# Performance work log

Hardware: AMD Instinct MI355X
Metric: run time of the kernel (lower is better)

The kernel has to match this reference:

```python
import jax, jax.numpy as jnp
import numpy as np

TAU = 2.0
V_TH = 1.0
ALPHA = 2.0  # ATan surrogate alpha (spikingjelly default)

@jax.custom_vjp
def atan_heaviside(x):
    # Forward: Heaviside spike; backward: ATan surrogate gradient.
    return (x >= 0).astype(x.dtype)

def _atan_fwd(x):
    return atan_heaviside(x), x

def _atan_bwd(x, g):
    sg = (ALPHA / 2.0) / (1.0 + (jnp.pi / 2.0 * ALPHA * x) ** 2)
    return (g * sg,)

atan_heaviside.defvjp(_atan_fwd, _atan_bwd)

def lif_scan(cur):
    # cur: [T, B, F] input currents. LIF: H = V + (X - V)/tau; S = H >= v_th; hard reset V = H*(1-S).
    def step(v, x_t):
        h = v + (x_t - v) / TAU
        s = atan_heaviside(h - V_TH)
        v_new = h * (1.0 - s)
        return v_new, s
    v0 = jnp.zeros(cur.shape[1:], dtype=cur.dtype)
    _, spikes = jax.lax.scan(step, v0, cur)
    return spikes

def setup_inputs() -> dict:
    key = jax.random.key(0)
    k1, k2 = jax.random.split(key)
    T, B, F_in, F_out = 64, 256, 1024, 1024
    x = jax.random.normal(k1, (T, B, F_in), dtype=jnp.float32)
    W = jax.random.normal(k2, (F_out, F_in), dtype=jnp.float32) * (1.0 / np.sqrt(F_in))
    return {"x": x, "W": W}

def reference(x, W):
    # Linear projection over all timesteps, then multi-step LIF recurrence.
    cur = jnp.einsum('tbf,of->tbo', x, W)  # [T, B, F_out]
    return lif_scan(cur)
```

## Files before the change

kernel.cpp:

```cpp
#include <hip/hip_runtime.h>


#define T_DIM 64
#define B_DIM 256
#define F_DIM 1024
#define K_DIM 1024
#define M_DIM 16384
#define COLS  (B_DIM * F_DIM)
#define KP    2048
#define MARGIN 6e-5f
#define LIST_CAP 32768

typedef __attribute__((ext_vector_type(8))) short short8;
typedef __attribute__((ext_vector_type(4))) float floatx4;

#define ASYNC_CP16(gp, lp)                                                     \
    __builtin_amdgcn_global_load_lds(                                          \
        (const __attribute__((address_space(1))) unsigned int*)(gp),           \
        (__attribute__((address_space(3))) unsigned int*)(lp), 16, 0, 0)

__device__ inline unsigned short f32_to_bf16_rne(float f) {
    unsigned int u = __builtin_bit_cast(unsigned int, f);
    unsigned int r = (u + 0x7FFFu + ((u >> 16) & 1u)) >> 16;
    return (unsigned short)r;
}
__device__ inline float bf16_to_f32(unsigned short h) {
    unsigned int u = ((unsigned int)h) << 16;
    return __builtin_bit_cast(float, u);
}

__global__ __launch_bounds__(256) void split_kernel(
    const float* __restrict__ x, const float* __restrict__ Wm,
    unsigned short* __restrict__ A, unsigned short* __restrict__ B,
    unsigned int* __restrict__ counter)
{
    if (blockIdx.x == 0 && threadIdx.x == 0) *counter = 0;
    const int blk = blockIdx.x;
    const float* in;
    unsigned short* dst;
    int g;
    int orow;
    if (blk < 16384) {
        g = blk * 256 + threadIdx.x;
        int e = g * 4;
        int row = e >> 10;
        orow = ((row & 255) << 6) | (row >> 8);
        in = x; dst = A;
    } else {
        g = (blk - 16384) * 256 + threadIdx.x;
        int e = g * 4;
        orow = e >> 10;
        in = Wm; dst = B;
    }
    int k = (g * 4) & 1023;
    float4 v = reinterpret_cast<const float4*>(in)[g];
    ushort4 h, l;
    float f;
    f = v.x; h.x = f32_to_bf16_rne(f); l.x = f32_to_bf16_rne(f - bf16_to_f32(h.x));
    f = v.y; h.y = f32_to_bf16_rne(f); l.y = f32_to_bf16_rne(f - bf16_to_f32(h.y));
    f = v.z; h.z = f32_to_bf16_rne(f); l.z = f32_to_bf16_rne(f - bf16_to_f32(h.z));
    f = v.w; h.w = f32_to_bf16_rne(f); l.w = f32_to_bf16_rne(f - bf16_to_f32(h.w));
    reinterpret_cast<ushort4*>(dst)[(size_t)orow * (KP / 4) + (k >> 2)] = h;
    reinterpret_cast<ushort4*>(dst)[(size_t)orow * (KP / 4) + 256 + (k >> 2)] = l;
}

__global__ __launch_bounds__(256, 2) void gemm_scan_kernel(
    const unsigned short* __restrict__ A,
    const unsigned short* __restrict__ B,
    float* __restrict__ out,
    unsigned int* __restrict__ counter, unsigned int* __restrict__ list)
{
    __shared__ unsigned short As[128 * 32];
    __shared__ unsigned short Bs[256 * 32];

    const int tid  = threadIdx.x;
    const int lane = tid & 63;
    const int wv   = tid >> 6;
    const int lid = blockIdx.x;
    const int mt  = ((lid & 7) << 4) | (lid >> 5);
    const int nt  = (lid >> 3) & 3;
    const int m0  = mt * 128;
    const int n0  = nt * 256;
    const int wm  = (wv & 1) * 64;
    const int wn  = (wv >> 1) * 128;

    floatx4 acc[4][8] = {};

    const int srow = tid >> 2;
    const int slin = (tid & 3) * 8;
    const int ssw  = (((tid & 3) ^ ((tid >> 3) & 3)) * 8);
    const int lrow = lane & 15;
    const int q    = lane >> 4;
    const int rsw  = (lrow >> 1) & 3;

    const unsigned short* Ab = A + (size_t)m0 * KP;
    const unsigned short* Bb = B + (size_t)n0 * KP;

    for (int k0 = 0; k0 < 3072; k0 += 32) {
        const int aoff = (k0 < 2048) ? k0 : k0 - 2048;
        const int boff = (k0 < 1024) ? k0 : k0 - 1024;
        __syncthreads();
        ASYNC_CP16(Ab + (size_t)srow * KP + aoff + ssw,         As + srow * 32 + slin);
        ASYNC_CP16(Ab + (size_t)(srow + 64) * KP + aoff + ssw,  As + (srow + 64) * 32 + slin);
        ASYNC_CP16(Bb + (size_t)srow * KP + boff + ssw,         Bs + srow * 32 + slin);
        ASYNC_CP16(Bb + (size_t)(srow + 64) * KP + boff + ssw,  Bs + (srow + 64) * 32 + slin);
        ASYNC_CP16(Bb + (size_t)(srow + 128) * KP + boff + ssw, Bs + (srow + 128) * 32 + slin);
        ASYNC_CP16(Bb + (size_t)(srow + 192) * KP + boff + ssw, Bs + (srow + 192) * 32 + slin);
        __syncthreads();

        const int sl = (q ^ rsw) * 8;
        short8 a[4], b[8];
#pragma unroll
        for (int i = 0; i < 4; ++i)
            a[i] = *reinterpret_cast<const short8*>(&As[(wm + i * 16 + lrow) * 32 + sl]);
#pragma unroll
        for (int j = 0; j < 8; ++j)
            b[j] = *reinterpret_cast<const short8*>(&Bs[(wn + j * 16 + lrow) * 32 + sl]);
#pragma unroll
        for (int i = 0; i < 4; ++i)
#pragma unroll
            for (int j = 0; j < 8; ++j)
                acc[i][j] = __builtin_amdgcn_mfma_f32_16x16x32_bf16(a[i], b[j], acc[i][j], 0, 0, 0);
    }

    const int col = lane & 15;
    const int b_g = mt * 2 + (wv & 1);

    unsigned int fmask = 0;
#pragma unroll
    for (int j = 0; j < 8; ++j) {
        float v = 0.f;
        bool fl = false;
#pragma unroll
        for (int i = 0; i < 4; ++i) {
#pragma unroll
            for (int qq = 0; qq < 4; ++qq) {
                if (q == qq) {
#pragma unroll
                    for (int r = 0; r < 4; ++r) {
                        float cu = acc[i][j][r];
                        float h = v + (cu - v) * 0.5f;
                        float d = h - 1.0f;
                        bool sp = (d >= 0.f);
                        fl |= (fabsf(d) < MARGIN);
                        acc[i][j][r] = sp ? 1.0f : 0.0f;
                        v = sp ? 0.f : h;
                    }
                }
                v = __shfl(v, qq * 16 + col, 64);
            }
        }
        if (fl) fmask |= (1u << j);
    }
    fmask |= __shfl_xor(fmask, 16, 64);
    fmask |= __shfl_xor(fmask, 32, 64);

    float* outp = out + (size_t)b_g * F_DIM;
#pragma unroll
    for (int i = 0; i < 4; ++i)
#pragma unroll
        for (int j = 0; j < 8; ++j)
#pragma unroll
            for (int r = 0; r < 4; ++r) {
                int t = i * 16 + q * 4 + r;
                int o = n0 + wn + j * 16 + col;
                outp[(size_t)t * COLS + o] = acc[i][j][r];
            }

    if (q == 0 && fmask) {
        for (int j = 0; j < 8; ++j)
            if (fmask & (1u << j)) {
                unsigned int idx = atomicAdd(counter, 1u);
                if (idx < LIST_CAP)
                    list[idx] = (unsigned int)((b_g << 10) | (n0 + wn + j * 16 + col));
            }
    }
}

__global__ __launch_bounds__(256) void fixup_kernel(
    const float* __restrict__ x, const float* __restrict__ W,
    const unsigned int* __restrict__ counter, const unsigned int* __restrict__ list,
    float* __restrict__ out)
{
    __shared__ double curd[T_DIM];
    __shared__ float wrow[K_DIM];
    unsigned int n = *counter;
    if (n > LIST_CAP) n = LIST_CAP;
    const int wv = threadIdx.x >> 6, lane = threadIdx.x & 63;

    for (unsigned int idx = blockIdx.x; idx < n; idx += gridDim.x) {
        const unsigned int c = list[idx];
        const int b = c >> 10, o = c & 1023;
        __syncthreads();
        for (int k = threadIdx.x; k < K_DIM; k += 256) wrow[k] = W[(size_t)o * K_DIM + k];
        __syncthreads();
        for (int it = 0; it < 16; ++it) {
            const int t = it * 4 + wv;
            const float* xp = x + (size_t)t * COLS + (size_t)b * F_DIM + lane * 16;
            double s = 0.0;
#pragma unroll
            for (int qq = 0; qq < 4; ++qq) {
                float4 xv = reinterpret_cast<const float4*>(xp)[qq];
                float4 wq = *reinterpret_cast<const float4*>(&wrow[lane * 16 + qq * 4]);
                s += (double)xv.x * (double)wq.x + (double)xv.y * (double)wq.y +
                     (double)xv.z * (double)wq.z + (double)xv.w * (double)wq.w;
            }
#pragma unroll
            for (int off = 32; off > 0; off >>= 1) s += __shfl_down(s, off, 64);
            if (lane == 0) curd[t] = s;
        }
        __syncthreads();
        if (threadIdx.x == 0) {
            double v = 0.0;
            for (int t = 0; t < T_DIM; ++t) {
                double h = v + (curd[t] - v) * 0.5;
                bool s = (h >= 1.0);
                out[(size_t)t * COLS + c] = s ? 1.0f : 0.0f;
                v = s ? 0.0 : h;
            }
        }
        __syncthreads();
    }
}

#define TILE 64
#define KC 32
#define XS_LD 36
#define SC_LD 65

__global__ __launch_bounds__(256) void lif_fused_kernel(
    const float* __restrict__ x, const float* __restrict__ Wm, float* __restrict__ out)
{
    __shared__ __align__(16) unsigned char smem_raw[TILE * SC_LD * sizeof(double)];
    float* sf = reinterpret_cast<float*>(smem_raw);
    double* sd = reinterpret_cast<double*>(smem_raw);
    float* Xs = sf;
    float* Ws = sf + TILE * XS_LD;

    const int b = blockIdx.y;
    const int o0 = blockIdx.x * TILE;
    const int tid = threadIdx.x;
    const int tx = tid & 15, ty = tid >> 4;

    double acc[4][4];
#pragma unroll
    for (int i = 0; i < 4; ++i)
#pragma unroll
        for (int j = 0; j < 4; ++j) acc[i][j] = 0.0;

    const int r = tid >> 3, c4 = (tid & 7) * 4;
    const float* xbase = x + (size_t)b * F_DIM;

    for (int k0 = 0; k0 < K_DIM; k0 += KC) {
        __syncthreads();
        float4 xv0 = *reinterpret_cast<const float4*>(xbase + (size_t)r * COLS + k0 + c4);
        float4 xv1 = *reinterpret_cast<const float4*>(xbase + (size_t)(r + 32) * COLS + k0 + c4);
        *reinterpret_cast<float4*>(Xs + r * XS_LD + c4) = xv0;
        *reinterpret_cast<float4*>(Xs + (r + 32) * XS_LD + c4) = xv1;
        float4 wv0 = *reinterpret_cast<const float4*>(Wm + (size_t)(o0 + r) * K_DIM + k0 + c4);
        float4 wv1 = *reinterpret_cast<const float4*>(Wm + (size_t)(o0 + r + 32) * K_DIM + k0 + c4);
        *reinterpret_cast<float4*>(Ws + r * XS_LD + c4) = wv0;
        *reinterpret_cast<float4*>(Ws + (r + 32) * XS_LD + c4) = wv1;
        __syncthreads();
#pragma unroll 4
        for (int kk = 0; kk < KC; ++kk) {
            double xa[4], wb[4];
#pragma unroll
            for (int i = 0; i < 4; ++i) xa[i] = (double)Xs[(4 * ty + i) * XS_LD + kk];
#pragma unroll
            for (int j = 0; j < 4; ++j) wb[j] = (double)Ws[(4 * tx + j) * XS_LD + kk];
#pragma unroll
            for (int i = 0; i < 4; ++i)
#pragma unroll
                for (int j = 0; j < 4; ++j) acc[i][j] = fma(xa[i], wb[j], acc[i][j]);
        }
    }
    __syncthreads();
#pragma unroll
    for (int i = 0; i < 4; ++i)
#pragma unroll
        for (int j = 0; j < 4; ++j) sd[(4 * ty + i) * SC_LD + (4 * tx + j)] = acc[i][j];
    __syncthreads();
    if (tid < TILE) {
        double v = 0.0;
        float* outp = out + (size_t)b * F_DIM + o0 + tid;
        for (int t = 0; t < T_DIM; ++t) {
            double cu = sd[t * SC_LD + tid];
            double h = v + (cu - v) * 0.5;
            bool s = (h >= 1.0);
            outp[(size_t)t * COLS] = s ? 1.0f : 0.0f;
            v = s ? 0.0 : h;
        }
    }
}

extern "C" void kernel_launch(void* const* d_in, const int* in_sizes, int n_in,
                              void* d_out, int out_size, void* d_ws, size_t ws_size,
                              hipStream_t stream) {
    const float* x = (const float*)d_in[0];
    const float* Wm = (const float*)d_in[1];
    float* out = (float*)d_out;

    const size_t OFF_A   = 0;
    const size_t OFF_B   = OFF_A + (size_t)M_DIM * KP * 2;
    const size_t OFF_CNT = OFF_B + (size_t)F_DIM * KP * 2;
    const size_t OFF_LST = OFF_CNT + 256;
    const size_t NEEDED  = OFF_LST + (size_t)LIST_CAP * 4;

    if (ws_size < NEEDED) {
        dim3 grid(F_DIM / TILE, B_DIM, 1);
        lif_fused_kernel<<<grid, dim3(256), 0, stream>>>(x, Wm, out);
        return;
    }

    unsigned char* ws = (unsigned char*)d_ws;
    unsigned short* Abuf = (unsigned short*)(ws + OFF_A);
    unsigned short* Bbuf = (unsigned short*)(ws + OFF_B);
    unsigned int* counter = (unsigned int*)(ws + OFF_CNT);
    unsigned int* list = (unsigned int*)(ws + OFF_LST);

    split_kernel<<<dim3(16384 + 1024), dim3(256), 0, stream>>>(x, Wm, Abuf, Bbuf, counter);
    gemm_scan_kernel<<<dim3(512), dim3(256), 0, stream>>>(Abuf, Bbuf, out, counter, list);
    fixup_kernel<<<dim3(512), dim3(256), 0, stream>>>(x, Wm, counter, list, out);
}
```

Baseline: 247.9 us.

## Load hi/lo bf16 splits together per K-step to reuse tiles across 3 MFMA passes

The split-bf16 GEMM used to run three separate K sweeps (hi*hi, lo*hi, hi*lo), reloading tiles each time. It now loads the hi and lo halves of A and B into separate LDS buffers in one 1024-long K loop and issues all three MFMA products per step. This cuts the number of K iterations and barriers and reuses each loaded tile across products. In exchange it doubles LDS use per block and raises register pressure, which could hurt occupancy at launch_bounds(256,2).

New measurement: 225.9 us. -8.9%, faster.

```diff
diff --git a/kernel.cpp b/kernel.cpp
--- a/kernel.cpp
+++ b/kernel.cpp
@@ -70,8 +70,10 @@
     float* __restrict__ out,
     unsigned int* __restrict__ counter, unsigned int* __restrict__ list)
 {
-    __shared__ unsigned short As[128 * 32];
-    __shared__ unsigned short Bs[256 * 32];
+    __shared__ unsigned short Ah[128 * 32];
+    __shared__ unsigned short Al[128 * 32];
+    __shared__ unsigned short Bh[256 * 32];
+    __shared__ unsigned short Bl[256 * 32];
 
     const int tid  = threadIdx.x;
     const int lane = tid & 63;
@@ -96,31 +98,57 @@
     const unsigned short* Ab = A + (size_t)m0 * KP;
     const unsigned short* Bb = B + (size_t)n0 * KP;
 
-    for (int k0 = 0; k0 < 3072; k0 += 32) {
-        const int aoff = (k0 < 2048) ? k0 : k0 - 2048;
-        const int boff = (k0 < 1024) ? k0 : k0 - 1024;
-        __syncthreads();
-        ASYNC_CP16(Ab + (size_t)srow * KP + aoff + ssw,         As + srow * 32 + slin);
-        ASYNC_CP16(Ab + (size_t)(srow + 64) * KP + aoff + ssw,  As + (srow + 64) * 32 + slin);
-        ASYNC_CP16(Bb + (size_t)srow * KP + boff + ssw,         Bs + srow * 32 + slin);
-        ASYNC_CP16(Bb + (size_t)(srow + 64) * KP + boff + ssw,  Bs + (srow + 64) * 32 + slin);
-        ASYNC_CP16(Bb + (size_t)(srow + 128) * KP + boff + ssw, Bs + (srow + 128) * 32 + slin);
-        ASYNC_CP16(Bb + (size_t)(srow + 192) * KP + boff + ssw, Bs + (srow + 192) * 32 + slin);
+    for (int k0 = 0; k0 < 1024; k0 += 32) {
+        __syncthreads();
+        ASYNC_CP16(Ab + (size_t)srow * KP + k0 + ssw,                Ah + srow * 32 + slin);
+        ASYNC_CP16(Ab + (size_t)(srow + 64) * KP + k0 + ssw,         Ah + (srow + 64) * 32 + slin);
+        ASYNC_CP16(Ab + (size_t)srow * KP + 1024 + k0 + ssw,         Al + srow * 32 + slin);
+        ASYNC_CP16(Ab + (size_t)(srow + 64) * KP + 1024 + k0 + ssw,  Al + (srow + 64) * 32 + slin);
+        ASYNC_CP16(Bb + (size_t)srow * KP + k0 + ssw,                Bh + srow * 32 + slin);
+        ASYNC_CP16(Bb + (size_t)(srow + 64) * KP + k0 + ssw,         Bh + (srow + 64) * 32 + slin);
+        ASYNC_CP16(Bb + (size_t)(srow + 128) * KP + k0 + ssw,        Bh + (srow + 128) * 32 + slin);
+        ASYNC_CP16(Bb + (size_t)(srow + 192) * KP + k0 + ssw,        Bh + (srow + 192) * 32 + slin);
+        ASYNC_CP16(Bb + (size_t)srow * KP + 1024 + k0 + ssw,         Bl + srow * 32 + slin);
+        ASYNC_CP16(Bb + (size_t)(srow + 64) * KP + 1024 + k0 + ssw,  Bl + (srow + 64) * 32 + slin);
+        ASYNC_CP16(Bb + (size_t)(srow + 128) * KP + 1024 + k0 + ssw, Bl + (srow + 128) * 32 + slin);
+        ASYNC_CP16(Bb + (size_t)(srow + 192) * KP + 1024 + k0 + ssw, Bl + (srow + 192) * 32 + slin);
         __syncthreads();
 
         const int sl = (q ^ rsw) * 8;
-        short8 a[4], b[8];
-#pragma unroll
-        for (int i = 0; i < 4; ++i)
-            a[i] = *reinterpret_cast<const short8*>(&As[(wm + i * 16 + lrow) * 32 + sl]);
-#pragma unroll
-        for (int j = 0; j < 8; ++j)
-            b[j] = *reinterpret_cast<const short8*>(&Bs[(wn + j * 16 + lrow) * 32 + sl]);
-#pragma unroll
-        for (int i = 0; i < 4; ++i)
-#pragma unroll
-            for (int j = 0; j < 8; ++j)
-                acc[i][j] = __builtin_amdgcn_mfma_f32_16x16x32_bf16(a[i], b[j], acc[i][j], 0, 0, 0);
+        short8 ah[4], al[4];
+#pragma unroll
+        for (int i = 0; i < 4; ++i) {
+            ah[i] = *reinterpret_cast<const short8*>(&Ah[(wm + i * 16 + lrow) * 32 + sl]);
+            al[i] = *reinterpret_cast<const short8*>(&Al[(wm + i * 16 + lrow) * 32 + sl]);
+        }
+#pragma unroll
+        for (int jh = 0; jh < 2; ++jh) {
+            short8 bh[4], bl[4];
+#pragma unroll
+            for (int j4 = 0; j4 < 4; ++j4) {
+                const int jr = (wn + (jh * 4 + j4) * 16 + lrow) * 32 + sl;
+                bh[j4] = *reinterpret_cast<const short8*>(&Bh[jr]);
+                bl[j4] = *reinterpret_cast<const short8*>(&Bl[jr]);
+            }
+#pragma unroll
+            for (int i = 0; i < 4; ++i)
+#pragma unroll
+                for (int j4 = 0; j4 < 4; ++j4)
+                    acc[i][jh * 4 + j4] = __builtin_amdgcn_mfma_f32_16x16x32_bf16(
+                        ah[i], bh[j4], acc[i][jh * 4 + j4], 0, 0, 0);
+#pragma unroll
+            for (int i = 0; i < 4; ++i)
+#pragma unroll
+                for (int j4 = 0; j4 < 4; ++j4)
+                    acc[i][jh * 4 + j4] = __builtin_amdgcn_mfma_f32_16x16x32_bf16(
+                        al[i], bh[j4], acc[i][jh * 4 + j4], 0, 0, 0);
+#pragma unroll
+            for (int i = 0; i < 4; ++i)
+#pragma unroll
+                for (int j4 = 0; j4 < 4; ++j4)
+                    acc[i][jh * 4 + j4] = __builtin_amdgcn_mfma_f32_16x16x32_bf16(
+                        ah[i], bl[j4], acc[i][jh * 4 + j4], 0, 0, 0);
+        }
     }
 
     const int col = lane & 15;
```
